# Performance work log

Hardware: AMD Instinct MI355X
Metric: run time of the kernel (lower is better)

The kernel has to match this reference:

```python
import jax, jax.numpy as jnp
import numpy as np

N = 10000
E = 160000
F_IN = 64
HID = 128
HEADS = 8
NC = 3
NEG_SLOPE = 0.2
EPS = 1e-16


def setup_inputs() -> dict:
    key = jax.random.key(0)
    ks = jax.random.split(key, 12)
    p = lambda k, shape: jax.random.normal(k, shape, jnp.float32) * 0.1
    return {
        "x": jax.random.normal(ks[0], (N, F_IN), jnp.float32),
        "edge_index": jax.random.randint(ks[1], (2, E), 0, N),
        # conv1: F_IN -> 8 heads x 128, concat -> 1024
        "W1": p(ks[2], (F_IN, HEADS * HID)),
        "a_src1": p(ks[3], (HEADS, HID)),
        "a_dst1": p(ks[4], (HEADS, HID)),
        "b1": jnp.zeros((HEADS * HID,), jnp.float32),
        # conv2: 1024 -> 8 heads x 64, concat -> 512
        "W2": p(ks[5], (HEADS * HID, HEADS * (HID // 2))),
        "a_src2": p(ks[6], (HEADS, HID // 2)),
        "a_dst2": p(ks[7], (HEADS, HID // 2)),
        "b2": jnp.zeros((HEADS * (HID // 2),), jnp.float32),
        # conv3: 512 -> 1 head x 3, mean (concat=False)
        "W3": p(ks[8], (HEADS * (HID // 2), NC)),
        "a_src3": p(ks[9], (1, NC)),
        "a_dst3": p(ks[10], (1, NC)),
        "b3": jnp.zeros((NC,), jnp.float32),
    }


def gat_conv(x, src, dst, W, a_src, a_dst, b, concat):
    """PyG-style GATConv (eval mode, self-loops already in src/dst)."""
    n = x.shape[0]
    H, C = a_src.shape
    h = (x @ W).reshape(n, H, C)                      # [N, H, C]
    s_src = jnp.sum(h * a_src[None], axis=-1)         # [N, H]
    s_dst = jnp.sum(h * a_dst[None], axis=-1)         # [N, H]
    e = jax.nn.leaky_relu(s_src[src] + s_dst[dst], NEG_SLOPE)  # [E, H]
    # segment softmax over incoming edges per destination node
    m = jax.ops.segment_max(e, dst, num_segments=n)   # [N, H]
    ex = jnp.exp(e - m[dst])
    denom = jax.ops.segment_sum(ex, dst, num_segments=n)
    alpha = ex / (denom[dst] + EPS)                   # [E, H]
    msg = h[src] * alpha[:, :, None]                  # [E, H, C]
    out = jax.ops.segment_sum(msg, dst, num_segments=n)  # [N, H, C]
    out = out.reshape(n, H * C) if concat else out.mean(axis=1)
    return out + b


def reference(x, edge_index, W1, a_src1, a_dst1, b1, W2, a_src2, a_dst2, b2, W3, a_src3, a_dst3, b3):
    n = x.shape[0]
    loop = jnp.arange(n, dtype=edge_index.dtype)
    src = jnp.concatenate([edge_index[0], loop])
    dst = jnp.concatenate([edge_index[1], loop])
    h = gat_conv(x, src, dst, W1, a_src1, a_dst1, b1, True)
    h = jax.nn.elu(h)
    h = gat_conv(h, src, dst, W2, a_src2, a_dst2, b2, True)
    h = jax.nn.elu(h)
    h = gat_conv(h, src, dst, W3, a_src3, a_dst3, b3, False)
    return jax.nn.log_softmax(h, axis=1)
```

## Files before the change

### kernel.cpp

```cpp
#include <hip/hip_runtime.h>
#include <math.h>

#define NEG_SLOPE 0.2f
#define EPS_DEN 1e-16f

typedef __attribute__((ext_vector_type(8))) short bf16x8;
typedef __attribute__((ext_vector_type(4))) float f32x4;

__device__ inline void split2(float a, short& hi, short& lo) {
    unsigned u = __float_as_uint(a);
    unsigned uh = (u + 0x8000u) & 0xFFFF0000u;
    float fh = __uint_as_float(uh);
    hi = (short)(uh >> 16);
    float r = a - fh;
    lo = (short)((__float_as_uint(r) + 0x8000u) >> 16);
}

__device__ inline unsigned short f2bf(float f) {
    unsigned u = __float_as_uint(f);
    return (unsigned short)((u + 0x7FFFu + ((u >> 16) & 1u)) >> 16);
}
__device__ inline float bflo(unsigned u) { return __uint_as_float(u << 16); }
__device__ inline float bfhi(unsigned u) { return __uint_as_float(u & 0xFFFF0000u); }

__global__ void k_count(const int* __restrict__ ei, int E, int Nn, int* counts) {
    int e = blockIdx.x * blockDim.x + threadIdx.x;
    int ET = E + Nn;
    if (e >= ET) return;
    int d = (e < E) ? ei[E + e] : (e - E);
    atomicAdd(&counts[d], 1);
}

__global__ void k_scan(const int* __restrict__ counts, int Nn, int ET, int* __restrict__ row_off) {
    __shared__ int lds[256];
    int t = threadIdx.x;
    int chunk = (Nn + 255) / 256;
    int b0 = t * chunk, b1 = min(Nn, b0 + chunk);
    int s = 0;
    for (int i = b0; i < b1; i++) s += counts[i];
    lds[t] = s;
    __syncthreads();
    if (t == 0) {
        int run = 0;
        for (int i = 0; i < 256; i++) { int v = lds[i]; lds[i] = run; run += v; }
    }
    __syncthreads();
    int run = lds[t];
    for (int i = b0; i < b1; i++) { row_off[i] = run; run += counts[i]; }
    if (t == 0) row_off[Nn] = ET;
}

__global__ void k_scatter(const int* __restrict__ ei, int E, int Nn,
                          const int* __restrict__ row_off, int* cursor, int* __restrict__ col) {
    int e = blockIdx.x * blockDim.x + threadIdx.x;
    int ET = E + Nn;
    if (e >= ET) return;
    int d = (e < E) ? ei[E + e] : (e - E);
    int s = (e < E) ? ei[e] : (e - E);
    int pos = atomicAdd(&cursor[d], 1);
    col[row_off[d] + pos] = s;
}

__global__ void k_split_x(const float* __restrict__ x, short* __restrict__ A,
                          int M, int Mp, int K) {
    int i = blockIdx.x * blockDim.x + threadIdx.x;
    if (i >= Mp * K) return;
    int row = i / K, c = i - row * K;
    float v = (row < M) ? x[(size_t)row * K + c] : 0.f;
    short hi, lo;
    split2(v, hi, lo);
    A[(size_t)row * (2 * K) + c] = hi;
    A[(size_t)row * (2 * K) + K + c] = lo;
}

__global__ __launch_bounds__(256) void k_split_wt(const float* __restrict__ W,
                                                  short* __restrict__ Bt, int K, int N, int dup) {
    __shared__ float s[32][33];
    int k0 = blockIdx.x * 32, n0 = blockIdx.y * 32;
    int tx = threadIdx.x & 31, ty = threadIdx.x >> 5;
    for (int r = ty; r < 32; r += 8) s[r][tx] = W[(size_t)(k0 + r) * N + n0 + tx];
    __syncthreads();
    int ldbt = (1 + dup) * K;
    for (int r = ty; r < 32; r += 8) {
        float v = s[tx][r];
        unsigned u = __float_as_uint(v);
        short hi = (short)((u + 0x7FFFu + ((u >> 16) & 1u)) >> 16);
        size_t base = (size_t)(n0 + r) * ldbt + k0 + tx;
        Bt[base] = hi;
        if (dup) Bt[base + K] = hi;
    }
}

__global__ __launch_bounds__(256) void k_mfma64(const short* __restrict__ A,
                                                const short* __restrict__ B,
                                                unsigned short* __restrict__ C,
                                                int M, int N, int Ktot,
                                                int lda, int ldb) {
    __shared__ short As[64 * 32];
    __shared__ short Bs[64 * 32];
    int t = threadIdx.x;
    int lane = t & 63;
    int wid = t >> 6;

    int nbx = N >> 6;
    int nb = gridDim.x;
    int q = nb >> 3, r = nb & 7;
    int xcd = blockIdx.x & 7, pos = blockIdx.x >> 3;
    int L = (xcd < r ? xcd * (q + 1) : r * (q + 1) + (xcd - r) * q) + pos;
    int bn = (L % nbx) * 64;
    int bm = (L / nbx) * 64;

    int wm = (wid >> 1) * 32, wn = (wid & 1) * 32;
    int fr = lane & 15, kq = lane >> 4;

    int srow = t >> 2, sslot = t & 3;
    int sko = ((sslot ^ ((srow >> 1) & 3)) << 3);

    f32x4 acc[2][2] = {};

    for (int k0 = 0; k0 < Ktot; k0 += 32) {
        {
            const short* sa = A + (size_t)(bm + srow) * lda + k0 + sko;
            const short* sb = B + (size_t)(bn + srow) * ldb + k0 + sko;
            short* da = As + (size_t)(wid << 6) * 8;
            short* db = Bs + (size_t)(wid << 6) * 8;
            __builtin_amdgcn_global_load_lds((const __attribute__((address_space(1))) void*)sa,
                                             (__attribute__((address_space(3))) void*)da, 16, 0, 0);
            __builtin_amdgcn_global_load_lds((const __attribute__((address_space(1))) void*)sb,
                                             (__attribute__((address_space(3))) void*)db, 16, 0, 0);
        }
        __syncthreads();
        bf16x8 af[2], bfv[2];
        #pragma unroll
        for (int i = 0; i < 2; i++) {
            int rowa = wm + i * 16 + fr;
            int rowb = wn + i * 16 + fr;
            af[i]  = *(const bf16x8*)(As + rowa * 32 + ((kq ^ ((rowa >> 1) & 3)) << 3));
            bfv[i] = *(const bf16x8*)(Bs + rowb * 32 + ((kq ^ ((rowb >> 1) & 3)) << 3));
        }
        #pragma unroll
        for (int i = 0; i < 2; i++)
            #pragma unroll
            for (int j = 0; j < 2; j++)
                acc[i][j] = __builtin_amdgcn_mfma_f32_16x16x32_bf16(af[i], bfv[j], acc[i][j], 0, 0, 0);
        __syncthreads();
    }
    #pragma unroll
    for (int i = 0; i < 2; i++) {
        int rbase = bm + wm + i * 16 + kq * 4;
        #pragma unroll
        for (int j = 0; j < 2; j++) {
            int colc = bn + wn + j * 16 + fr;
            #pragma unroll
            for (int rg = 0; rg < 4; rg++) {
                int rr = rbase + rg;
                if (rr < M) C[(size_t)rr * N + colc] = f2bf(acc[i][j][rg]);
            }
        }
    }
}

template<int H, int C>
__global__ __launch_bounds__(256) void k_scores_bf(const unsigned short* __restrict__ h,
                                                   const float* __restrict__ a_src,
                                                   const float* __restrict__ a_dst,
                                                   float* __restrict__ ssrc,
                                                   float* __restrict__ sdst, int Nn) {
    constexpr int D = H * C;
    constexpr int PER = D / 64;
    constexpr int GRP = C / PER;
    int lane = threadIdx.x & 63;
    int n = blockIdx.x * 4 + (threadIdx.x >> 6);
    if (n >= Nn) return;
    const unsigned short* hp = h + (size_t)n * D + lane * PER;
    int cb = lane * PER;
    float as = 0.f, ad = 0.f;
    #pragma unroll
    for (int j0 = 0; j0 < PER; j0 += 8) {
        uint4 u = *(const uint4*)(hp + j0);
        int c = cb + j0;
        as += bflo(u.x) * a_src[c + 0] + bfhi(u.x) * a_src[c + 1]
            + bflo(u.y) * a_src[c + 2] + bfhi(u.y) * a_src[c + 3]
            + bflo(u.z) * a_src[c + 4] + bfhi(u.z) * a_src[c + 5]
            + bflo(u.w) * a_src[c + 6] + bfhi(u.w) * a_src[c + 7];
        ad += bflo(u.x) * a_dst[c + 0] + bfhi(u.x) * a_dst[c + 1]
            + bflo(u.y) * a_dst[c + 2] + bfhi(u.y) * a_dst[c + 3]
            + bflo(u.z) * a_dst[c + 4] + bfhi(u.z) * a_dst[c + 5]
            + bflo(u.w) * a_dst[c + 6] + bfhi(u.w) * a_dst[c + 7];
    }
    #pragma unroll
    for (int off = GRP >> 1; off >= 1; off >>= 1) {
        as += __shfl_xor(as, off);
        ad += __shfl_xor(ad, off);
    }
    if ((lane & (GRP - 1)) == 0) {
        int hh = lane / GRP;
        ssrc[n * H + hh] = as;
        sdst[n * H + hh] = ad;
    }
}

__global__ __launch_bounds__(256) void k_gemm_n3s(const float* __restrict__ A, const float* __restrict__ W,
                                                  const float* __restrict__ as3, const float* __restrict__ ad3,
                                                  float* __restrict__ C3, float* __restrict__ ssrc,
                                                  float* __restrict__ sdst, int M, int K) {
    __shared__ float lw[1536];
    int t = threadIdx.x;
    for (int i = t; i < K * 3; i += 256) lw[i] = W[i];
    __syncthreads();
    int lane = t & 63;
    int n = blockIdx.x * 4 + (t >> 6);
    if (n >= M) return;
    float a0 = 0.f, a1 = 0.f, a2 = 0.f;
    for (int c = lane; c < K; c += 64) {
        float v = A[(size_t)n * K + c];
        a0 += v * lw[c * 3 + 0];
        a1 += v * lw[c * 3 + 1];
        a2 += v * lw[c * 3 + 2];
    }
    #pragma unroll
    for (int off = 32; off > 0; off >>= 1) {
        a0 += __shfl_xor(a0, off);
        a1 += __shfl_xor(a1, off);
        a2 += __shfl_xor(a2, off);
    }
    if (lane == 0) {
        C3[n * 3 + 0] = a0; C3[n * 3 + 1] = a1; C3[n * 3 + 2] = a2;
        ssrc[n] = a0 * as3[0] + a1 * as3[1] + a2 * as3[2];
        sdst[n] = a0 * ad3[0] + a1 * ad3[1] + a2 * ad3[2];
    }
}

template<int H, int C, int CB, bool ELU, bool BFOUT>
__global__ __launch_bounds__(256) void k_agg_wv(const unsigned short* __restrict__ hsrc,
                                                const float* __restrict__ ssrc,
                                                const float* __restrict__ sdst,
                                                const int* __restrict__ col,
                                                const int* __restrict__ row_off,
                                                const float* __restrict__ bias,
                                                float* __restrict__ out,
                                                unsigned short* __restrict__ osp) {
    constexpr int D = H * C;
    int lane = threadIdx.x & 63;
    int w = blockIdx.x * 4 + (threadIdx.x >> 6);
    if (w >= 10000 * CB) {}
    int n, cb;
    if (CB == 2) { n = w >> 1; cb = w & 1; } else { n = w; cb = 0; }
    int col0 = cb * 512 + lane * 8;
    int myhead = col0 / C;
    float sd = sdst[n * H + myhead];
    int beg = row_off[n], end = row_off[n + 1];
    const unsigned short* hbase = hsrc + col0;

    float acc[8] = {0.f, 0.f, 0.f, 0.f, 0.f, 0.f, 0.f, 0.f};
    float den = 0.f;
    #pragma unroll 2
    for (int j = beg; j < end; j++) {
        int cj = col[j];
        float s = ssrc[cj * H + myhead] + sd;
        s = (s >= 0.f) ? s : NEG_SLOPE * s;
        float ex = __expf(s);
        den += ex;
        uint4 u = *(const uint4*)(hbase + (size_t)cj * D);
        acc[0] += ex * bflo(u.x); acc[1] += ex * bfhi(u.x);
        acc[2] += ex * bflo(u.y); acc[3] += ex * bfhi(u.y);
        acc[4] += ex * bflo(u.z); acc[5] += ex * bfhi(u.z);
        acc[6] += ex * bflo(u.w); acc[7] += ex * bfhi(u.w);
    }
    float iv = 1.f / (den + EPS_DEN);
    float vals[8];
    #pragma unroll
    for (int v = 0; v < 8; v++) {
        float val = acc[v] * iv + bias[col0 + v];
        if (ELU) val = (val > 0.f) ? val : (__expf(val) - 1.f);
        vals[v] = val;
    }
    if (BFOUT) {
        uint4 o;
        o.x = (unsigned)f2bf(vals[0]) | ((unsigned)f2bf(vals[1]) << 16);
        o.y = (unsigned)f2bf(vals[2]) | ((unsigned)f2bf(vals[3]) << 16);
        o.z = (unsigned)f2bf(vals[4]) | ((unsigned)f2bf(vals[5]) << 16);
        o.w = (unsigned)f2bf(vals[6]) | ((unsigned)f2bf(vals[7]) << 16);
        *(uint4*)(osp + (size_t)n * D + col0) = o;
    } else {
        *(f32x4*)(out + (size_t)n * D + col0) = *(f32x4*)&vals[0];
        *(f32x4*)(out + (size_t)n * D + col0 + 4) = *(f32x4*)&vals[4];
    }
}

template<int H, int C, int CB, bool ELU, bool BFOUT>
__global__ __launch_bounds__(256) void k_agg_wave(const unsigned short* __restrict__ hsrc,
                                                  const float* __restrict__ ssrc,
                                                  const float* __restrict__ sdst,
                                                  const int* __restrict__ col,
                                                  const int* __restrict__ row_off,
                                                  const float* __restrict__ bias,
                                                  float* __restrict__ out,
                                                  unsigned short* __restrict__ osp,
                                                  int nw) {
    constexpr int D = H * C;
    int lane = threadIdx.x & 63;
    int w = blockIdx.x * 4 + (threadIdx.x >> 6);
    if (w >= nw) return;
    int n, cb;
    if (CB == 2) { n = w >> 1; cb = w & 1; } else { n = w; cb = 0; }
    int col0 = cb * 512 + lane * 8;
    int myhead = col0 / C;
    float sd = sdst[n * H + myhead];
    int beg = row_off[n], end = row_off[n + 1];
    const unsigned short* hbase = hsrc + col0;

    float acc[8] = {0.f, 0.f, 0.f, 0.f, 0.f, 0.f, 0.f, 0.f};
    float den = 0.f;
    #pragma unroll 2
    for (int j = beg; j < end; j++) {
        int cj = col[j];
        float s = ssrc[cj * H + myhead] + sd;
        s = (s >= 0.f) ? s : NEG_SLOPE * s;
        float ex = __expf(s);
        den += ex;
        uint4 u = *(const uint4*)(hbase + (size_t)cj * D);
        acc[0] += ex * bflo(u.x); acc[1] += ex * bfhi(u.x);
        acc[2] += ex * bflo(u.y); acc[3] += ex * bfhi(u.y);
        acc[4] += ex * bflo(u.z); acc[5] += ex * bfhi(u.z);
        acc[6] += ex * bflo(u.w); acc[7] += ex * bfhi(u.w);
    }
    float iv = 1.f / (den + EPS_DEN);
    float vals[8];
    #pragma unroll
    for (int v = 0; v < 8; v++) {
        float val = acc[v] * iv + bias[col0 + v];
        if (ELU) val = (val > 0.f) ? val : (__expf(val) - 1.f);
        vals[v] = val;
    }
    if (BFOUT) {
        uint4 o;
        o.x = (unsigned)f2bf(vals[0]) | ((unsigned)f2bf(vals[1]) << 16);
        o.y = (unsigned)f2bf(vals[2]) | ((unsigned)f2bf(vals[3]) << 16);
        o.z = (unsigned)f2bf(vals[4]) | ((unsigned)f2bf(vals[5]) << 16);
        o.w = (unsigned)f2bf(vals[6]) | ((unsigned)f2bf(vals[7]) << 16);
        *(uint4*)(osp + (size_t)n * D + col0) = o;
    } else {
        *(f32x4*)(out + (size_t)n * D + col0) = *(f32x4*)&vals[0];
        *(f32x4*)(out + (size_t)n * D + col0 + 4) = *(f32x4*)&vals[4];
    }
}

__global__ void k_l3_fused(const float* __restrict__ h3, const float* __restrict__ ssrc,
                           const float* __restrict__ sdst, const int* __restrict__ col,
                           const int* __restrict__ row_off, const float* __restrict__ b3,
                           float* __restrict__ out, int Nn) {
    int n = blockIdx.x * blockDim.x + threadIdx.x;
    if (n >= Nn) return;
    int beg = row_off[n], end = row_off[n + 1];
    float sd = sdst[n];
    float den = 0.f, a0 = 0.f, a1 = 0.f, a2 = 0.f;
    for (int j = beg; j < end; j++) {
        int sI = col[j];
        float s = ssrc[sI] + sd;
        s = (s >= 0.f) ? s : NEG_SLOPE * s;
        float ex = __expf(s);
        den += ex;
        a0 += ex * h3[sI * 3 + 0];
        a1 += ex * h3[sI * 3 + 1];
        a2 += ex * h3[sI * 3 + 2];
    }
    float iv = 1.f / (den + EPS_DEN);
    float v0 = a0 * iv + b3[0], v1 = a1 * iv + b3[1], v2 = a2 * iv + b3[2];
    float m = fmaxf(v0, fmaxf(v1, v2));
    float l = logf(__expf(v0 - m) + __expf(v1 - m) + __expf(v2 - m));
    out[n * 3 + 0] = v0 - m - l;
    out[n * 3 + 1] = v1 - m - l;
    out[n * 3 + 2] = v2 - m - l;
}

extern "C" void kernel_launch(void* const* d_in, const int* in_sizes, int n_in,
                              void* d_out, int out_size, void* d_ws, size_t ws_size,
                              hipStream_t stream) {
    (void)n_in; (void)out_size; (void)ws_size;
    const float* x   = (const float*)d_in[0];
    const int*   ei  = (const int*)d_in[1];
    const float* W1  = (const float*)d_in[2];
    const float* as1 = (const float*)d_in[3];
    const float* ad1 = (const float*)d_in[4];
    const float* b1  = (const float*)d_in[5];
    const float* W2  = (const float*)d_in[6];
    const float* as2 = (const float*)d_in[7];
    const float* ad2 = (const float*)d_in[8];
    const float* b2  = (const float*)d_in[9];
    const float* W3  = (const float*)d_in[10];
    const float* as3 = (const float*)d_in[11];
    const float* ad3 = (const float*)d_in[12];
    const float* b3  = (const float*)d_in[13];
    float* out = (float*)d_out;

    const int Nn = in_sizes[0] / 64;
    const int E  = in_sizes[1] / 2;
    const int ET = E + Nn;
    const int Mp = ((Nn + 127) / 128) * 128;

    char* ws = (char*)d_ws;
    size_t off = 0;
    auto alloc = [&](size_t bytes) -> void* {
        void* p = ws + off;
        off = (off + bytes + 255) & ~(size_t)255;
        return p;
    };
    unsigned short* hbuf = (unsigned short*)alloc((size_t)Mp * 1024 * 2);
    void*  big  = alloc((size_t)Mp * 1024 * 2 + 65536);
    unsigned short* A2 = (unsigned short*)big;
    float* obuf = (float*)big;
    float* h3   = (float*)alloc((size_t)Nn * 3 * 4);
    short* A1   = (short*)alloc((size_t)Mp * 128 * 2);
    short* B1t  = (short*)alloc((size_t)1024 * 128 * 2);
    short* B2t  = (short*)alloc((size_t)512 * 1024 * 2);
    float* ssrc = (float*)alloc((size_t)Nn * 8 * 4);
    float* sdst = (float*)alloc((size_t)Nn * 8 * 4);
    int* counts = (int*)alloc((size_t)Nn * 2 * 4);
    int* cursor = counts + Nn;
    int* row_off= (int*)alloc((size_t)(Nn + 1) * 4);
    int* colb   = (int*)alloc((size_t)ET * 4);

    hipMemsetAsync(counts, 0, (size_t)Nn * 2 * 4, stream);

    int etb = (ET + 255) / 256;
    k_count<<<etb, 256, 0, stream>>>(ei, E, Nn, counts);
    k_scan<<<1, 256, 0, stream>>>(counts, Nn, ET, row_off);
    k_scatter<<<etb, 256, 0, stream>>>(ei, E, Nn, row_off, cursor, colb);

    k_split_x<<<(Mp * 64 + 255) / 256, 256, 0, stream>>>(x, A1, Nn, Mp, 64);
    k_split_wt<<<dim3(64 / 32, 1024 / 32), 256, 0, stream>>>(W1, B1t, 64, 1024, 1);
    k_split_wt<<<dim3(1024 / 32, 512 / 32), 256, 0, stream>>>(W2, B2t, 1024, 512, 0);

    {
        int nb = (1024 / 64) * (Mp / 64);
        k_mfma64<<<nb, 256, 0, stream>>>(A1, B1t, hbuf, Nn, 1024, 128, 128, 128);
        k_scores_bf<8, 128><<<(Nn + 3) / 4, 256, 0, stream>>>(hbuf, as1, ad1, ssrc, sdst, Nn);
        int nw = Nn * 2;
        k_agg_wave<8, 128, 2, true, true><<<(nw + 3) / 4, 256, 0, stream>>>(hbuf, ssrc, sdst, colb, row_off, b1, nullptr, A2, nw);
    }
    {
        int nb = (512 / 64) * (Mp / 64);
        k_mfma64<<<nb, 256, 0, stream>>>((const short*)A2, B2t, hbuf, Nn, 512, 1024, 1024, 1024);
        k_scores_bf<8, 64><<<(Nn + 3) / 4, 256, 0, stream>>>(hbuf, as2, ad2, ssrc, sdst, Nn);
        int nw = Nn;
        k_agg_wave<8, 64, 1, true, false><<<(nw + 3) / 4, 256, 0, stream>>>(hbuf, ssrc, sdst, colb, row_off, b2, obuf, nullptr, nw);
    }
    {
        k_gemm_n3s<<<(Nn + 3) / 4, 256, 0, stream>>>(obuf, W3, as3, ad3, h3, ssrc, sdst, Nn, 512);
        k_l3_fused<<<(Nn + 255) / 256, 256, 0, stream>>>(h3, ssrc, sdst, colb, row_off, b3, out, Nn);
    }
}
```

Measured before the change: 199.3 us.

## Fuse layer-2 scores into GEMM epilogue and layer-3 projection into aggregation

New measurement: 190.3 us. 1.05x faster.

```diff
diff --git a/kernel.cpp b/kernel.cpp
--- a/kernel.cpp
+++ b/kernel.cpp
@@ -40,12 +40,14 @@
     for (int i = b0; i < b1; i++) s += counts[i];
     lds[t] = s;
     __syncthreads();
-    if (t == 0) {
-        int run = 0;
-        for (int i = 0; i < 256; i++) { int v = lds[i]; lds[i] = run; run += v; }
-    }
-    __syncthreads();
-    int run = lds[t];
+    #pragma unroll
+    for (int d = 1; d < 256; d <<= 1) {
+        int v = (t >= d) ? lds[t - d] : 0;
+        __syncthreads();
+        lds[t] += v;
+        __syncthreads();
+    }
+    int run = (t == 0) ? 0 : lds[t - 1];
     for (int i = b0; i < b1; i++) { row_off[i] = run; run += counts[i]; }
     if (t == 0) row_off[Nn] = ET;
 }
@@ -91,13 +93,19 @@
     }
 }
 
+template<bool FUSESC>
 __global__ __launch_bounds__(256) void k_mfma64(const short* __restrict__ A,
                                                 const short* __restrict__ B,
                                                 unsigned short* __restrict__ C,
+                                                const float* __restrict__ a_src,
+                                                const float* __restrict__ a_dst,
+                                                float* __restrict__ ssrc,
+                                                float* __restrict__ sdst,
                                                 int M, int N, int Ktot,
                                                 int lda, int ldb) {
     __shared__ short As[64 * 32];
     __shared__ short Bs[64 * 32];
+    __shared__ float sred[4][64][2];
     int t = threadIdx.x;
     int lane = t & 63;
     int wid = t >> 6;
@@ -156,6 +164,57 @@
                 int rr = rbase + rg;
                 if (rr < M) C[(size_t)rr * N + colc] = f2bf(acc[i][j][rg]);
             }
+        }
+    }
+    if (FUSESC) {
+        float asv[2], adv[2];
+        #pragma unroll
+        for (int j = 0; j < 2; j++) {
+            int colc = bn + wn + j * 16 + fr;
+            asv[j] = a_src[colc];
+            adv[j] = a_dst[colc];
+        }
+        float ps[8], pd[8];
+        #pragma unroll
+        for (int i = 0; i < 2; i++)
+            #pragma unroll
+            for (int rg = 0; rg < 4; rg++) {
+                int k8 = i * 4 + rg;
+                ps[k8] = acc[i][0][rg] * asv[0] + acc[i][1][rg] * asv[1];
+                pd[k8] = acc[i][0][rg] * adv[0] + acc[i][1][rg] * adv[1];
+            }
+        #pragma unroll
+        for (int k8 = 0; k8 < 8; k8++) {
+            #pragma unroll
+            for (int off = 1; off < 16; off <<= 1) {
+                ps[k8] += __shfl_xor(ps[k8], off);
+                pd[k8] += __shfl_xor(pd[k8], off);
+            }
+        }
+        if (fr == 0) {
+            #pragma unroll
+            for (int i = 0; i < 2; i++)
+                #pragma unroll
+                for (int rg = 0; rg < 4; rg++) {
+                    int rl = wm + i * 16 + kq * 4 + rg;
+                    sred[wid][rl][0] = ps[i * 4 + rg];
+                    sred[wid][rl][1] = pd[i * 4 + rg];
+                }
+        }
+        __syncthreads();
+        if ((wid & 1) == 0 && fr == 0) {
+            int hh = bn >> 6;
+            #pragma unroll
+            for (int i = 0; i < 2; i++)
+                #pragma unroll
+                for (int rg = 0; rg < 4; rg++) {
+                    int rl = wm + i * 16 + kq * 4 + rg;
+                    int rr = bm + rl;
+                    if (rr < M) {
+                        ssrc[rr * 8 + hh] = sred[wid][rl][0] + sred[wid | 1][rl][0];
+                        sdst[rr * 8 + hh] = sred[wid][rl][1] + sred[wid | 1][rl][1];
+                    }
+                }
         }
     }
 }
@@ -197,94 +256,6 @@
         int hh = lane / GRP;
         ssrc[n * H + hh] = as;
         sdst[n * H + hh] = ad;
-    }
-}
-
-__global__ __launch_bounds__(256) void k_gemm_n3s(const float* __restrict__ A, const float* __restrict__ W,
-                                                  const float* __restrict__ as3, const float* __restrict__ ad3,
-                                                  float* __restrict__ C3, float* __restrict__ ssrc,
-                                                  float* __restrict__ sdst, int M, int K) {
-    __shared__ float lw[1536];
-    int t = threadIdx.x;
-    for (int i = t; i < K * 3; i += 256) lw[i] = W[i];
-    __syncthreads();
-    int lane = t & 63;
-    int n = blockIdx.x * 4 + (t >> 6);
-    if (n >= M) return;
-    float a0 = 0.f, a1 = 0.f, a2 = 0.f;
-    for (int c = lane; c < K; c += 64) {
-        float v = A[(size_t)n * K + c];
-        a0 += v * lw[c * 3 + 0];
-        a1 += v * lw[c * 3 + 1];
-        a2 += v * lw[c * 3 + 2];
-    }
-    #pragma unroll
-    for (int off = 32; off > 0; off >>= 1) {
-        a0 += __shfl_xor(a0, off);
-        a1 += __shfl_xor(a1, off);
-        a2 += __shfl_xor(a2, off);
-    }
-    if (lane == 0) {
-        C3[n * 3 + 0] = a0; C3[n * 3 + 1] = a1; C3[n * 3 + 2] = a2;
-        ssrc[n] = a0 * as3[0] + a1 * as3[1] + a2 * as3[2];
-        sdst[n] = a0 * ad3[0] + a1 * ad3[1] + a2 * ad3[2];
-    }
-}
-
-template<int H, int C, int CB, bool ELU, bool BFOUT>
-__global__ __launch_bounds__(256) void k_agg_wv(const unsigned short* __restrict__ hsrc,
-                                                const float* __restrict__ ssrc,
-                                                const float* __restrict__ sdst,
-                                                const int* __restrict__ col,
-                                                const int* __restrict__ row_off,
-                                                const float* __restrict__ bias,
-                                                float* __restrict__ out,
-                                                unsigned short* __restrict__ osp) {
-    constexpr int D = H * C;
-    int lane = threadIdx.x & 63;
-    int w = blockIdx.x * 4 + (threadIdx.x >> 6);
-    if (w >= 10000 * CB) {}
-    int n, cb;
-    if (CB == 2) { n = w >> 1; cb = w & 1; } else { n = w; cb = 0; }
-    int col0 = cb * 512 + lane * 8;
-    int myhead = col0 / C;
-    float sd = sdst[n * H + myhead];
-    int beg = row_off[n], end = row_off[n + 1];
-    const unsigned short* hbase = hsrc + col0;
-
-    float acc[8] = {0.f, 0.f, 0.f, 0.f, 0.f, 0.f, 0.f, 0.f};
-    float den = 0.f;
-    #pragma unroll 2
-    for (int j = beg; j < end; j++) {
-        int cj = col[j];
-        float s = ssrc[cj * H + myhead] + sd;
-        s = (s >= 0.f) ? s : NEG_SLOPE * s;
-        float ex = __expf(s);
-        den += ex;
-        uint4 u = *(const uint4*)(hbase + (size_t)cj * D);
-        acc[0] += ex * bflo(u.x); acc[1] += ex * bfhi(u.x);
-        acc[2] += ex * bflo(u.y); acc[3] += ex * bfhi(u.y);
-        acc[4] += ex * bflo(u.z); acc[5] += ex * bfhi(u.z);
-        acc[6] += ex * bflo(u.w); acc[7] += ex * bfhi(u.w);
-    }
-    float iv = 1.f / (den + EPS_DEN);
-    float vals[8];
-    #pragma unroll
-    for (int v = 0; v < 8; v++) {
-        float val = acc[v] * iv + bias[col0 + v];
-        if (ELU) val = (val > 0.f) ? val : (__expf(val) - 1.f);
-        vals[v] = val;
-    }
-    if (BFOUT) {
-        uint4 o;
-        o.x = (unsigned)f2bf(vals[0]) | ((unsigned)f2bf(vals[1]) << 16);
-        o.y = (unsigned)f2bf(vals[2]) | ((unsigned)f2bf(vals[3]) << 16);
-        o.z = (unsigned)f2bf(vals[4]) | ((unsigned)f2bf(vals[5]) << 16);
-        o.w = (unsigned)f2bf(vals[6]) | ((unsigned)f2bf(vals[7]) << 16);
-        *(uint4*)(osp + (size_t)n * D + col0) = o;
-    } else {
-        *(f32x4*)(out + (size_t)n * D + col0) = *(f32x4*)&vals[0];
-        *(f32x4*)(out + (size_t)n * D + col0 + 4) = *(f32x4*)&vals[4];
     }
 }
 
@@ -346,6 +317,68 @@
     }
 }
 
+__global__ __launch_bounds__(256) void k_agg2_l3(const unsigned short* __restrict__ hsrc,
+                                                 const float* __restrict__ ssrc,
+                                                 const float* __restrict__ sdst,
+                                                 const int* __restrict__ col,
+                                                 const int* __restrict__ row_off,
+                                                 const float* __restrict__ bias,
+                                                 const float* __restrict__ W3,
+                                                 const float* __restrict__ as3,
+                                                 const float* __restrict__ ad3,
+                                                 float* __restrict__ h3,
+                                                 float* __restrict__ ssrc3,
+                                                 float* __restrict__ sdst3,
+                                                 int Nn) {
+    constexpr int D = 512;
+    int lane = threadIdx.x & 63;
+    int n = blockIdx.x * 4 + (threadIdx.x >> 6);
+    if (n >= Nn) return;
+    int col0 = lane * 8;
+    int myhead = lane >> 3;
+    float sd = sdst[n * 8 + myhead];
+    int beg = row_off[n], end = row_off[n + 1];
+    const unsigned short* hbase = hsrc + col0;
+
+    float acc[8] = {0.f, 0.f, 0.f, 0.f, 0.f, 0.f, 0.f, 0.f};
+    float den = 0.f;
+    #pragma unroll 2
+    for (int j = beg; j < end; j++) {
+        int cj = col[j];
+        float s = ssrc[cj * 8 + myhead] + sd;
+        s = (s >= 0.f) ? s : NEG_SLOPE * s;
+        float ex = __expf(s);
+        den += ex;
+        uint4 u = *(const uint4*)(hbase + (size_t)cj * D);
+        acc[0] += ex * bflo(u.x); acc[1] += ex * bfhi(u.x);
+        acc[2] += ex * bflo(u.y); acc[3] += ex * bfhi(u.y);
+        acc[4] += ex * bflo(u.z); acc[5] += ex * bfhi(u.z);
+        acc[6] += ex * bflo(u.w); acc[7] += ex * bfhi(u.w);
+    }
+    float iv = 1.f / (den + EPS_DEN);
+    float t0 = 0.f, t1 = 0.f, t2 = 0.f;
+    #pragma unroll
+    for (int v = 0; v < 8; v++) {
+        float val = acc[v] * iv + bias[col0 + v];
+        val = (val > 0.f) ? val : (__expf(val) - 1.f);
+        const float* wp = W3 + (size_t)(col0 + v) * 3;
+        t0 += val * wp[0];
+        t1 += val * wp[1];
+        t2 += val * wp[2];
+    }
+    #pragma unroll
+    for (int off = 32; off >= 1; off >>= 1) {
+        t0 += __shfl_xor(t0, off);
+        t1 += __shfl_xor(t1, off);
+        t2 += __shfl_xor(t2, off);
+    }
+    if (lane == 0) {
+        h3[n * 3 + 0] = t0; h3[n * 3 + 1] = t1; h3[n * 3 + 2] = t2;
+        ssrc3[n] = t0 * as3[0] + t1 * as3[1] + t2 * as3[2];
+        sdst3[n] = t0 * ad3[0] + t1 * ad3[1] + t2 * ad3[2];
+    }
+}
+
 __global__ void k_l3_fused(const float* __restrict__ h3, const float* __restrict__ ssrc,
                            const float* __restrict__ sdst, const int* __restrict__ col,
                            const int* __restrict__ row_off, const float* __restrict__ b3,
@@ -407,15 +440,17 @@
         return p;
     };
     unsigned short* hbuf = (unsigned short*)alloc((size_t)Mp * 1024 * 2);
-    void*  big  = alloc((size_t)Mp * 1024 * 2 + 65536);
-    unsigned short* A2 = (unsigned short*)big;
-    float* obuf = (float*)big;
+    unsigned short* A2   = (unsigned short*)alloc((size_t)Mp * 1024 * 2);
     float* h3   = (float*)alloc((size_t)Nn * 3 * 4);
     short* A1   = (short*)alloc((size_t)Mp * 128 * 2);
     short* B1t  = (short*)alloc((size_t)1024 * 128 * 2);
     short* B2t  = (short*)alloc((size_t)512 * 1024 * 2);
     float* ssrc = (float*)alloc((size_t)Nn * 8 * 4);
     float* sdst = (float*)alloc((size_t)Nn * 8 * 4);
+    float* ssrcB= (float*)alloc((size_t)Nn * 8 * 4);
+    float* sdstB= (float*)alloc((size_t)Nn * 8 * 4);
+    float* ssrc3= (float*)alloc((size_t)Nn * 4);
+    float* sdst3= (float*)alloc((size_t)Nn * 4);
     int* counts = (int*)alloc((size_t)Nn * 2 * 4);
     int* cursor = counts + Nn;
     int* row_off= (int*)alloc((size_t)(Nn + 1) * 4);
@@ -434,20 +469,19 @@
 
     {
         int nb = (1024 / 64) * (Mp / 64);
-        k_mfma64<<<nb, 256, 0, stream>>>(A1, B1t, hbuf, Nn, 1024, 128, 128, 128);
+        k_mfma64<false><<<nb, 256, 0, stream>>>(A1, B1t, hbuf, nullptr, nullptr, nullptr, nullptr,
+                                                Nn, 1024, 128, 128, 128);
         k_scores_bf<8, 128><<<(Nn + 3) / 4, 256, 0, stream>>>(hbuf, as1, ad1, ssrc, sdst, Nn);
         int nw = Nn * 2;
-        k_agg_wave<8, 128, 2, true, true><<<(nw + 3) / 4, 256, 0, stream>>>(hbuf, ssrc, sdst, colb, row_off, b1, nullptr, A2, nw);
+        k_agg_wave<8, 128, 2, true, true><<<(nw + 3) / 4, 256, 0, stream>>>(
+            hbuf, ssrc, sdst, colb, row_off, b1, nullptr, A2, nw);
     }
     {
         int nb = (512 / 64) * (Mp / 64);
-        k_mfma64<<<nb, 256, 0, stream>>>((const short*)A2, B2t, hbuf, Nn, 512, 1024, 1024, 1024);
-        k_scores_bf<8, 64><<<(Nn + 3) / 4, 256, 0, stream>>>(hbuf, as2, ad2, ssrc, sdst, Nn);
-        int nw = Nn;
-        k_agg_wave<8, 64, 1, true, false><<<(nw + 3) / 4, 256, 0, stream>>>(hbuf, ssrc, sdst, colb, row_off, b2, obuf, nullptr, nw);
-    }
-    {
-        k_gemm_n3s<<<(Nn + 3) / 4, 256, 0, stream>>>(obuf, W3, as3, ad3, h3, ssrc, sdst, Nn, 512);
-        k_l3_fused<<<(Nn + 255) / 256, 256, 0, stream>>>(h3, ssrc, sdst, colb, row_off, b3, out, Nn);
-    }
-}
+        k_mfma64<true><<<nb, 256, 0, stream>>>((const short*)A2, B2t, hbuf, as2, ad2, ssrcB, sdstB,
+                                               Nn, 512, 1024, 1024, 1024);
+        k_agg2_l3<<<(Nn + 3) / 4, 256, 0, stream>>>(hbuf, ssrcB, sdstB, colb, row_off, b2,
+                                                    W3, as3, ad3, h3, ssrc3, sdst3, Nn);
+    }
+    k_l3_fused<<<(Nn + 255) / 256, 256, 0, stream>>>(h3, ssrc3, sdst3, colb, row_off, b3, out, Nn);
+}
```
